# Kernel optimization log

Measured on AMD Instinct MI355X. Metric: run time of the kernel, lower is better.

The kernel has to match this reference:

```python
import jax, jax.numpy as jnp
import numpy as np
from jax import lax

MAX_DISP = 4  # correlation window radius -> 9x9 = 81 offsets


def setup_inputs() -> dict:
    key = jax.random.key(0)
    k1, k2 = jax.random.split(key)
    B, C, H, W = 4, 256, 128, 128
    x_1 = jax.random.normal(k1, (B, C, H, W), dtype=jnp.float32)
    x_2 = jax.random.normal(k2, (B, C, H, W), dtype=jnp.float32)
    return {"x_1": x_1, "x_2": x_2}


def reference(x_1, x_2):
    # FlowNet-style correlation: for each displacement (dy, dx) in [-4, 4]^2,
    # out[b, (dy+4)*9 + (dx+4), y, x] = mean_c x1[b,c,y,x] * x2[b,c,y+dy,x+dx]
    # with zero padding of x2 (normalized by C, as in the original CUDA kernel).
    B, C, H, W = x_1.shape
    pad = jnp.pad(x_2, ((0, 0), (0, 0), (MAX_DISP, MAX_DISP), (MAX_DISP, MAX_DISP)))
    outs = []
    for dy in range(2 * MAX_DISP + 1):
        for dx in range(2 * MAX_DISP + 1):
            shifted = lax.dynamic_slice(pad, (0, 0, dy, dx), (B, C, H, W))
            outs.append(jnp.mean(x_1 * shifted, axis=1))  # [B, H, W]
    return jnp.stack(outs, axis=1)  # [B, 81, H, W]
```

## Files before the change

kernel.cpp:

```cpp
#include <hip/hip_runtime.h>


#define MD 4
constexpr int Bc = 4, Cc = 256, Hc = 128, Wc = 128;
constexpr int TH = 16, TW = 16;
constexpr int NDY = 3;
constexpr int CC = 4;
constexpr int SROWS = TH + NDY - 1;
constexpr int SCOLS = TW + 2 * MD;
constexpr int RSC = 48;
constexpr int CH_STRIDE = SROWS * RSC;
constexpr int BUF_DW = CC * CH_STRIDE;
constexpr int NF4 = CC * SROWS * (SCOLS / 4);
constexpr int NTHR = 192;
constexpr int NSLOT = 3;
constexpr int NK = Cc / CC;

__global__ __launch_bounds__(NTHR, 4)
void corr_kernel(const float* __restrict__ x1, const float* __restrict__ x2,
                 float* __restrict__ out)
{
    __shared__ float stg[2 * BUF_DW];

    const int tid  = threadIdx.x;
    const int w    = tid >> 6;
    const int lane = tid & 63;
    const int gy   = lane >> 2;
    const int gx   = lane & 3;

    const int bid  = blockIdx.x;
    const int q    = bid / 24;
    const int r    = bid - q * 24;
    const int g    = r >> 3;
    const int t    = q * 8 + (r & 7);
    const int tx = t & 7;
    const int ty = (t >> 3) & 7;
    const int bb = t >> 6;
    const int x0 = tx * TW, y0 = ty * TH;
    const int rowbase = y0 + 3 * g - MD;

    int  s_goff[NSLOT], s_loff[NSLOT];
    bool s_val[NSLOT], s_act[NSLOT];
    #pragma unroll
    for (int s = 0; s < NSLOT; ++s) {
        int idx = tid + s * NTHR;
        bool active = idx < NF4;
        int i2  = active ? idx : 0;
        int cl  = i2 / (SROWS * 6);
        int rem = i2 - cl * (SROWS * 6);
        int rr  = rem / 6;
        int gc  = rem - rr * 6;
        int yy  = rowbase + rr;
        int xx  = x0 - 4 + 4 * gc;
        s_act[s]  = active;
        s_val[s]  = active && ((unsigned)yy < (unsigned)Hc) && ((unsigned)xx < (unsigned)(Wc - 3));
        s_goff[s] = cl * (Hc * Wc) + yy * Wc + xx;
        s_loff[s] = cl * CH_STRIDE + rr * RSC + 4 * gc;
    }

    const float* x2b = x2 + (size_t)bb * Cc * Hc * Wc;
    const float* x1b = x1 + (((size_t)bb * Cc) * Hc + (y0 + gy)) * Wc + x0 + 4 * gx;

    float acc[9][4];
    #pragma unroll
    for (int dx = 0; dx < 9; ++dx)
        #pragma unroll
        for (int p = 0; p < 4; ++p) acc[dx][p] = 0.f;

    const float4 f40 = make_float4(0.f, 0.f, 0.f, 0.f);
    float4 nf[NSLOT];

    #pragma unroll
    for (int s = 0; s < NSLOT; ++s) {
        nf[s] = f40;
        if (s_val[s]) nf[s] = *(const float4*)(x2b + s_goff[s]);
    }
    #pragma unroll
    for (int s = 0; s < NSLOT; ++s)
        if (s_act[s]) *(float4*)(&stg[s_loff[s]]) = nf[s];

    for (int k = 0; k < NK; ++k) {
        const int pb = k & 1;
        __syncthreads();
        if (k + 1 < NK) {
            const int gof = (k + 1) * CC * Hc * Wc;
            #pragma unroll
            for (int s = 0; s < NSLOT; ++s) {
                nf[s] = f40;
                if (s_val[s]) nf[s] = *(const float4*)(x2b + gof + s_goff[s]);
            }
        }
        #pragma unroll
        for (int cl = 0; cl < CC; ++cl) {
            const int c = k * CC + cl;
            const float4 a4 = *(const float4*)(x1b + c * (Hc * Wc));
            const float* rowp = &stg[pb * BUF_DW + cl * CH_STRIDE + (gy + w) * RSC + 4 * gx];
            const float4 q0 = *(const float4*)(rowp);
            const float4 q1 = *(const float4*)(rowp + 4);
            const float4 q2 = *(const float4*)(rowp + 8);
            const float v[12] = {q0.x, q0.y, q0.z, q0.w,
                                 q1.x, q1.y, q1.z, q1.w,
                                 q2.x, q2.y, q2.z, q2.w};
            const float a[4] = {a4.x, a4.y, a4.z, a4.w};
            #pragma unroll
            for (int dx = 0; dx < 9; ++dx)
                #pragma unroll
                for (int p = 0; p < 4; ++p)
                    acc[dx][p] += a[p] * v[dx + p];
        }
        if (k + 1 < NK) {
            const int lb = ((k + 1) & 1) * BUF_DW;
            #pragma unroll
            for (int s = 0; s < NSLOT; ++s)
                if (s_act[s]) *(float4*)(&stg[lb + s_loff[s]]) = nf[s];
        }
    }

    const float inv = 1.0f / (float)Cc;
    float* ob = out + (((size_t)bb * 81 + (3 * g + w) * 9) * Hc + (y0 + gy)) * Wc + x0 + 4 * gx;
    #pragma unroll
    for (int dx = 0; dx < 9; ++dx) {
        float4 st = make_float4(acc[dx][0] * inv, acc[dx][1] * inv,
                                acc[dx][2] * inv, acc[dx][3] * inv);
        *(float4*)(ob + dx * (Hc * Wc)) = st;
    }
}

extern "C" void kernel_launch(void* const* d_in, const int* in_sizes, int n_in,
                              void* d_out, int out_size, void* d_ws, size_t ws_size,
                              hipStream_t stream) {
    const float* x1 = (const float*)d_in[0];
    const float* x2 = (const float*)d_in[1];
    float* out = (float*)d_out;
    dim3 grid(3 * 8 * 8 * Bc), block(NTHR);
    corr_kernel<<<grid, block, 0, stream>>>(x1, x2, out);
}
```

Baseline: 201.7 us.

## Split channel reduction across two blocks and widen per-thread tile to 8 pixels

Each thread now computes 8 output pixels instead of 4 (tile width 32), which raises register reuse of the shared-memory x2 row. The channel dimension is split in two halves processed by separate blocks that write partial results to workspace, and a second reduce kernel sums them and applies the 1/C scale. The channel chunk per iteration is halved and the barrier is moved after the global prefetch issue. This keeps the grid the same size while raising per-thread work. The cost is extra partial-output traffic (two full 81-channel buffers written and read again) plus a second launch.

```diff
diff --git a/kernel.cpp b/kernel.cpp
--- a/kernel.cpp
+++ b/kernel.cpp
@@ -3,22 +3,23 @@
 
 #define MD 4
 constexpr int Bc = 4, Cc = 256, Hc = 128, Wc = 128;
-constexpr int TH = 16, TW = 16;
+constexpr int HW = Hc * Wc;
+constexpr int TH = 16, TW = 32;
 constexpr int NDY = 3;
-constexpr int CC = 4;
+constexpr int CC = 2;
 constexpr int SROWS = TH + NDY - 1;
 constexpr int SCOLS = TW + 2 * MD;
-constexpr int RSC = 48;
+constexpr int RSC = 44;
 constexpr int CH_STRIDE = SROWS * RSC;
 constexpr int BUF_DW = CC * CH_STRIDE;
 constexpr int NF4 = CC * SROWS * (SCOLS / 4);
 constexpr int NTHR = 192;
-constexpr int NSLOT = 3;
-constexpr int NK = Cc / CC;
+constexpr int NSLOT = 2;
+constexpr long long OUTNLL = (long long)Bc * 81 * HW;
 
-__global__ __launch_bounds__(NTHR, 4)
+__global__ __launch_bounds__(NTHR, 3)
 void corr_kernel(const float* __restrict__ x1, const float* __restrict__ x2,
-                 float* __restrict__ out)
+                 float* __restrict__ dst, int nh, float scl)
 {
     __shared__ float stg[2 * BUF_DW];
 
@@ -33,11 +34,16 @@
     const int r    = bid - q * 24;
     const int g    = r >> 3;
     const int t    = q * 8 + (r & 7);
-    const int tx = t & 7;
-    const int ty = (t >> 3) & 7;
-    const int bb = t >> 6;
+    const int tx   = t & 3;
+    const int ty   = (t >> 2) & 7;
+    const int rest = t >> 5;
+    const int hh   = (nh == 2) ? (rest & 1) : 0;
+    const int bb   = (nh == 2) ? (rest >> 1) : rest;
     const int x0 = tx * TW, y0 = ty * TH;
     const int rowbase = y0 + 3 * g - MD;
+    const int CN = Cc / nh;
+    const int NK = CN / CC;
+    const int c0 = hh * CN;
 
     int  s_goff[NSLOT], s_loff[NSLOT];
     bool s_val[NSLOT], s_act[NSLOT];
@@ -46,26 +52,26 @@
         int idx = tid + s * NTHR;
         bool active = idx < NF4;
         int i2  = active ? idx : 0;
-        int cl  = i2 / (SROWS * 6);
-        int rem = i2 - cl * (SROWS * 6);
-        int rr  = rem / 6;
-        int gc  = rem - rr * 6;
+        int cl  = i2 / (SROWS * 10);
+        int rem = i2 - cl * (SROWS * 10);
+        int rr  = rem / 10;
+        int gc  = rem - rr * 10;
         int yy  = rowbase + rr;
         int xx  = x0 - 4 + 4 * gc;
         s_act[s]  = active;
         s_val[s]  = active && ((unsigned)yy < (unsigned)Hc) && ((unsigned)xx < (unsigned)(Wc - 3));
-        s_goff[s] = cl * (Hc * Wc) + yy * Wc + xx;
+        s_goff[s] = cl * HW + yy * Wc + xx;
         s_loff[s] = cl * CH_STRIDE + rr * RSC + 4 * gc;
     }
 
-    const float* x2b = x2 + (size_t)bb * Cc * Hc * Wc;
-    const float* x1b = x1 + (((size_t)bb * Cc) * Hc + (y0 + gy)) * Wc + x0 + 4 * gx;
+    const float* x2b = x2 + ((size_t)bb * Cc + c0) * HW;
+    const float* x1b = x1 + ((size_t)bb * Cc + c0) * HW + (y0 + gy) * Wc + x0 + 8 * gx;
 
-    float acc[9][4];
+    float acc[9][8];
     #pragma unroll
     for (int dx = 0; dx < 9; ++dx)
         #pragma unroll
-        for (int p = 0; p < 4; ++p) acc[dx][p] = 0.f;
+        for (int p = 0; p < 8; ++p) acc[dx][p] = 0.f;
 
     const float4 f40 = make_float4(0.f, 0.f, 0.f, 0.f);
     float4 nf[NSLOT];
@@ -81,31 +87,33 @@
 
     for (int k = 0; k < NK; ++k) {
         const int pb = k & 1;
-        __syncthreads();
         if (k + 1 < NK) {
-            const int gof = (k + 1) * CC * Hc * Wc;
+            const int gof = (k + 1) * CC * HW;
             #pragma unroll
             for (int s = 0; s < NSLOT; ++s) {
                 nf[s] = f40;
                 if (s_val[s]) nf[s] = *(const float4*)(x2b + gof + s_goff[s]);
             }
         }
+        __syncthreads();
         #pragma unroll
         for (int cl = 0; cl < CC; ++cl) {
             const int c = k * CC + cl;
-            const float4 a4 = *(const float4*)(x1b + c * (Hc * Wc));
-            const float* rowp = &stg[pb * BUF_DW + cl * CH_STRIDE + (gy + w) * RSC + 4 * gx];
+            const float* xp = x1b + (size_t)c * HW;
+            const float4 a0 = *(const float4*)(xp);
+            const float4 a1 = *(const float4*)(xp + 4);
+            const float* rowp = &stg[pb * BUF_DW + cl * CH_STRIDE + (gy + w) * RSC + 8 * gx];
             const float4 q0 = *(const float4*)(rowp);
             const float4 q1 = *(const float4*)(rowp + 4);
             const float4 q2 = *(const float4*)(rowp + 8);
-            const float v[12] = {q0.x, q0.y, q0.z, q0.w,
-                                 q1.x, q1.y, q1.z, q1.w,
-                                 q2.x, q2.y, q2.z, q2.w};
-            const float a[4] = {a4.x, a4.y, a4.z, a4.w};
+            const float4 q3 = *(const float4*)(rowp + 12);
+            const float v[16] = {q0.x, q0.y, q0.z, q0.w,  q1.x, q1.y, q1.z, q1.w,
+                                 q2.x, q2.y, q2.z, q2.w,  q3.x, q3.y, q3.z, q3.w};
+            const float a[8] = {a0.x, a0.y, a0.z, a0.w,  a1.x, a1.y, a1.z, a1.w};
             #pragma unroll
             for (int dx = 0; dx < 9; ++dx)
                 #pragma unroll
-                for (int p = 0; p < 4; ++p)
+                for (int p = 0; p < 8; ++p)
                     acc[dx][p] += a[p] * v[dx + p];
         }
         if (k + 1 < NK) {
@@ -116,13 +124,32 @@
         }
     }
 
-    const float inv = 1.0f / (float)Cc;
-    float* ob = out + (((size_t)bb * 81 + (3 * g + w) * 9) * Hc + (y0 + gy)) * Wc + x0 + 4 * gx;
+    float* ob = dst + (size_t)hh * OUTNLL
+              + (((size_t)bb * 81 + (3 * g + w) * 9) * Hc + (y0 + gy)) * Wc + x0 + 8 * gx;
     #pragma unroll
     for (int dx = 0; dx < 9; ++dx) {
-        float4 st = make_float4(acc[dx][0] * inv, acc[dx][1] * inv,
-                                acc[dx][2] * inv, acc[dx][3] * inv);
-        *(float4*)(ob + dx * (Hc * Wc)) = st;
+        float4 s0 = make_float4(acc[dx][0] * scl, acc[dx][1] * scl,
+                                acc[dx][2] * scl, acc[dx][3] * scl);
+        float4 s1 = make_float4(acc[dx][4] * scl, acc[dx][5] * scl,
+                                acc[dx][6] * scl, acc[dx][7] * scl);
+        *(float4*)(ob + dx * HW)     = s0;
+        *(float4*)(ob + dx * HW + 4) = s1;
+    }
+}
+
+__global__ __launch_bounds__(256)
+void reduce_kernel(const float* __restrict__ ws, float* __restrict__ out, float scl)
+{
+    const long long N4 = OUTNLL / 4;
+    const float4* pa = (const float4*)ws;
+    const float4* pb = (const float4*)(ws + OUTNLL);
+    float4* po = (float4*)out;
+    long long i = (long long)blockIdx.x * 256 + threadIdx.x;
+    const long long step = (long long)gridDim.x * 256;
+    for (; i < N4; i += step) {
+        float4 a = pa[i], b = pb[i];
+        po[i] = make_float4((a.x + b.x) * scl, (a.y + b.y) * scl,
+                            (a.z + b.z) * scl, (a.w + b.w) * scl);
     }
 }
 
@@ -132,6 +159,15 @@
     const float* x1 = (const float*)d_in[0];
     const float* x2 = (const float*)d_in[1];
     float* out = (float*)d_out;
-    dim3 grid(3 * 8 * 8 * Bc), block(NTHR);
-    corr_kernel<<<grid, block, 0, stream>>>(x1, x2, out);
+    const float inv = 1.0f / (float)Cc;
+    const size_t need = (size_t)(2 * OUTNLL) * sizeof(float);
+    if (d_ws != nullptr && ws_size >= need) {
+        float* ws = (float*)d_ws;
+        dim3 grid(24 * 32), block(NTHR);
+        corr_kernel<<<grid, block, 0, stream>>>(x1, x2, ws, 2, 1.0f);
+        reduce_kernel<<<dim3(2048), dim3(256), 0, stream>>>(ws, out, inv);
+    } else {
+        dim3 grid(24 * 16), block(NTHR);
+        corr_kernel<<<grid, block, 0, stream>>>(x1, x2, out, 1, inv);
+    }
 }
```

After: 204.9 us. No clear change (+1.6%).

## Split channel reduction across two block halves with workspace partials and reduce pass

Applied to the files above, without the earlier changes.

Splits the 256-channel reduction into two halves so twice as many blocks (1536 instead of 768) run, each writing partial correlations to a workspace, then a second kernel sums the two partials and applies the 1/C scale. This targets low occupancy and poor latency hiding on a grid that was small relative to the GPU's CU count. It adds about 2x the output size in extra global writes and reads plus a second launch. It also moves the barrier after the next-chunk global loads are issued so those loads overlap the wait.

```diff
diff --git a/kernel.cpp b/kernel.cpp
--- a/kernel.cpp
+++ b/kernel.cpp
@@ -3,6 +3,7 @@
 
 #define MD 4
 constexpr int Bc = 4, Cc = 256, Hc = 128, Wc = 128;
+constexpr int HW = Hc * Wc;
 constexpr int TH = 16, TW = 16;
 constexpr int NDY = 3;
 constexpr int CC = 4;
@@ -14,11 +15,11 @@
 constexpr int NF4 = CC * SROWS * (SCOLS / 4);
 constexpr int NTHR = 192;
 constexpr int NSLOT = 3;
-constexpr int NK = Cc / CC;
+constexpr long long OUTN = (long long)Bc * 81 * HW;
 
 __global__ __launch_bounds__(NTHR, 4)
 void corr_kernel(const float* __restrict__ x1, const float* __restrict__ x2,
-                 float* __restrict__ out)
+                 float* __restrict__ dst, int nh, float scl)
 {
     __shared__ float stg[2 * BUF_DW];
 
@@ -32,12 +33,17 @@
     const int q    = bid / 24;
     const int r    = bid - q * 24;
     const int g    = r >> 3;
-    const int t    = q * 8 + (r & 7);
+    const int tp   = q * 8 + (r & 7);
+    const int hh   = (nh == 2) ? (tp >> 8) : 0;
+    const int t    = tp & 255;
     const int tx = t & 7;
     const int ty = (t >> 3) & 7;
     const int bb = t >> 6;
     const int x0 = tx * TW, y0 = ty * TH;
     const int rowbase = y0 + 3 * g - MD;
+    const int CN = Cc / nh;
+    const int NK = CN / CC;
+    const int c0 = hh * CN;
 
     int  s_goff[NSLOT], s_loff[NSLOT];
     bool s_val[NSLOT], s_act[NSLOT];
@@ -54,12 +60,12 @@
         int xx  = x0 - 4 + 4 * gc;
         s_act[s]  = active;
         s_val[s]  = active && ((unsigned)yy < (unsigned)Hc) && ((unsigned)xx < (unsigned)(Wc - 3));
-        s_goff[s] = cl * (Hc * Wc) + yy * Wc + xx;
+        s_goff[s] = cl * HW + yy * Wc + xx;
         s_loff[s] = cl * CH_STRIDE + rr * RSC + 4 * gc;
     }
 
-    const float* x2b = x2 + (size_t)bb * Cc * Hc * Wc;
-    const float* x1b = x1 + (((size_t)bb * Cc) * Hc + (y0 + gy)) * Wc + x0 + 4 * gx;
+    const float* x2b = x2 + ((size_t)bb * Cc + c0) * HW;
+    const float* x1b = x1 + ((size_t)bb * Cc + c0) * HW + (y0 + gy) * Wc + x0 + 4 * gx;
 
     float acc[9][4];
     #pragma unroll
@@ -81,19 +87,19 @@
 
     for (int k = 0; k < NK; ++k) {
         const int pb = k & 1;
-        __syncthreads();
         if (k + 1 < NK) {
-            const int gof = (k + 1) * CC * Hc * Wc;
+            const int gof = (k + 1) * CC * HW;
             #pragma unroll
             for (int s = 0; s < NSLOT; ++s) {
                 nf[s] = f40;
                 if (s_val[s]) nf[s] = *(const float4*)(x2b + gof + s_goff[s]);
             }
         }
+        __syncthreads();
         #pragma unroll
         for (int cl = 0; cl < CC; ++cl) {
             const int c = k * CC + cl;
-            const float4 a4 = *(const float4*)(x1b + c * (Hc * Wc));
+            const float4 a4 = *(const float4*)(x1b + (size_t)c * HW);
             const float* rowp = &stg[pb * BUF_DW + cl * CH_STRIDE + (gy + w) * RSC + 4 * gx];
             const float4 q0 = *(const float4*)(rowp);
             const float4 q1 = *(const float4*)(rowp + 4);
@@ -116,13 +122,29 @@
         }
     }
 
-    const float inv = 1.0f / (float)Cc;
-    float* ob = out + (((size_t)bb * 81 + (3 * g + w) * 9) * Hc + (y0 + gy)) * Wc + x0 + 4 * gx;
+    float* ob = dst + (size_t)hh * OUTN
+              + (((size_t)bb * 81 + (3 * g + w) * 9) * Hc + (y0 + gy)) * Wc + x0 + 4 * gx;
     #pragma unroll
     for (int dx = 0; dx < 9; ++dx) {
-        float4 st = make_float4(acc[dx][0] * inv, acc[dx][1] * inv,
-                                acc[dx][2] * inv, acc[dx][3] * inv);
-        *(float4*)(ob + dx * (Hc * Wc)) = st;
+        float4 st = make_float4(acc[dx][0] * scl, acc[dx][1] * scl,
+                                acc[dx][2] * scl, acc[dx][3] * scl);
+        *(float4*)(ob + dx * HW) = st;
+    }
+}
+
+__global__ __launch_bounds__(256)
+void reduce_kernel(const float* __restrict__ ws, float* __restrict__ out, float scl)
+{
+    const long long N4 = OUTN / 4;
+    const float4* pa = (const float4*)ws;
+    const float4* pb = (const float4*)(ws + OUTN);
+    float4* po = (float4*)out;
+    long long i = (long long)blockIdx.x * 256 + threadIdx.x;
+    const long long step = (long long)gridDim.x * 256;
+    for (; i < N4; i += step) {
+        float4 a = pa[i], b = pb[i];
+        po[i] = make_float4((a.x + b.x) * scl, (a.y + b.y) * scl,
+                            (a.z + b.z) * scl, (a.w + b.w) * scl);
     }
 }
 
@@ -132,6 +154,15 @@
     const float* x1 = (const float*)d_in[0];
     const float* x2 = (const float*)d_in[1];
     float* out = (float*)d_out;
-    dim3 grid(3 * 8 * 8 * Bc), block(NTHR);
-    corr_kernel<<<grid, block, 0, stream>>>(x1, x2, out);
+    const float inv = 1.0f / (float)Cc;
+    const size_t need = (size_t)(2 * OUTN) * sizeof(float);
+    if (d_ws != nullptr && ws_size >= need) {
+        float* ws = (float*)d_ws;
+        dim3 grid(24 * 64), block(NTHR);
+        corr_kernel<<<grid, block, 0, stream>>>(x1, x2, ws, 2, 1.0f);
+        reduce_kernel<<<dim3(2048), dim3(256), 0, stream>>>(ws, out, inv);
+    } else {
+        dim3 grid(24 * 32), block(NTHR);
+        corr_kernel<<<grid, block, 0, stream>>>(x1, x2, out, 1, inv);
+    }
 }
```

Result: slower. 230.6 us (+14.4%).
